# Kernel tuning notes

Measured on AMD Instinct MI355X. Metric: run time of the kernel, lower is better.

Reference implementation:

```python
import jax, jax.numpy as jnp
import numpy as np

N_NODES = 100000
N_EDGES = 1600000
N_FEAT = 128
HIDDEN = 128
N_CLASSES = 40


def gcn_conv(x, W, b, src, dst, norm, n):
    # PyG GCNConv: linear (no bias) -> gather src -> scale by sym norm -> scatter-add to dst -> + bias
    h = x @ W                      # [N, out]
    m = h[src] * norm[:, None]     # [E+N, out] gathered, normalized messages
    out = jax.ops.segment_sum(m, dst, num_segments=n)
    return out + b


def setup_inputs() -> dict:
    key = jax.random.key(0)
    ks = jax.random.split(key, 10)
    x = jax.random.normal(ks[0], (N_NODES, N_FEAT), dtype=jnp.float32)
    edge_index = jax.random.randint(ks[1], (2, N_EDGES), 0, N_NODES, dtype=jnp.int32)

    def lin(k, fan_in, fan_out):
        s = 1.0 / np.sqrt(fan_in)
        return (jax.random.uniform(k, (fan_in, fan_out), jnp.float32, -s, s))

    return {
        "x": x,
        "edge_index": edge_index,
        "W1": lin(ks[2], N_FEAT, HIDDEN), "b1": jnp.zeros((HIDDEN,), jnp.float32),
        "W2": lin(ks[3], HIDDEN, HIDDEN), "b2": jnp.zeros((HIDDEN,), jnp.float32),
        "W3": lin(ks[4], HIDDEN, HIDDEN), "b3": jnp.zeros((HIDDEN,), jnp.float32),
        "W4": lin(ks[5], HIDDEN, N_CLASSES), "b4": jnp.zeros((N_CLASSES,), jnp.float32),
    }


def reference(x, edge_index, W1, b1, W2, b2, W3, b3, W4, b4):
    n = x.shape[0]
    # add self-loops (PyG GCNConv default)
    loops = jnp.arange(n, dtype=edge_index.dtype)
    src = jnp.concatenate([edge_index[0], loops])
    dst = jnp.concatenate([edge_index[1], loops])
    # symmetric degree normalization: deg computed on destination index
    deg = jax.ops.segment_sum(jnp.ones_like(dst, x.dtype), dst, num_segments=n)
    dinv = jnp.where(deg > 0, jax.lax.rsqrt(deg), 0.0)
    norm = dinv[src] * dinv[dst]

    h = jax.nn.relu(gcn_conv(x, W1, b1, src, dst, norm, n))   # dropout = identity (eval)
    h = jax.nn.relu(gcn_conv(h, W2, b2, src, dst, norm, n))
    h = jax.nn.relu(gcn_conv(h, W3, b3, src, dst, norm, n))
    x_latent = h
    out = gcn_conv(h, W4, b4, src, dst, norm, n)
    return out, x_latent
```

## Files before the change

### kernel.cpp

```cpp
#include <hip/hip_runtime.h>
#include <hip/hip_bf16.h>
#include <hip/hip_fp16.h>


#define N_NODES 100000
#define N_EDGES 1600000

#define BSHIFT 7
#define BWIDTH 128
#define CELL_CAP 512
#define P1_EPT 16
#define P1_CHUNK 4096

typedef short s16x8 __attribute__((ext_vector_type(8)));
typedef _Float16 f16x8 __attribute__((ext_vector_type(8)));
typedef float f32x4 __attribute__((ext_vector_type(4)));
typedef float f32x2 __attribute__((ext_vector_type(2)));


__global__ void init_aux(int* __restrict__ bcur2, int* __restrict__ spillCnt, int m) {
    int i = blockIdx.x * blockDim.x + threadIdx.x;
    if (i < m) bcur2[i] = 0;
    if (i == 0) *spillCnt = 0;
}

__global__ __launch_bounds__(256) void pass1_bucket(const int* __restrict__ src,
                                                    const int* __restrict__ dst,
                                                    int* __restrict__ bcur2,
                                                    int2* __restrict__ cells,
                                                    int2* __restrict__ spill,
                                                    int* __restrict__ spillCnt,
                                                    int nb, int e) {
    __shared__ int hist[1024];
    __shared__ int base[1024];
    int t = threadIdx.x;
    int x = blockIdx.x & 7;
    int e0 = blockIdx.x * P1_CHUNK;

    for (int i = t; i < nb; i += 256) hist[i] = 0;
    __syncthreads();

    int ds[P1_EPT], ss[P1_EPT];
#pragma unroll
    for (int j = 0; j < P1_EPT; j++) {
        int i = e0 + j * 256 + t;
        if (i < e) {
            ds[j] = dst[i];
            ss[j] = src[i];
            atomicAdd(&hist[ds[j] >> BSHIFT], 1);
        } else {
            ds[j] = -1;
        }
    }
    __syncthreads();

    for (int i = t; i < nb; i += 256) {
        int h = hist[i];
        base[i] = (h > 0) ? atomicAdd(&bcur2[i * 8 + x], h) : 0;
        hist[i] = 0;
    }
    __syncthreads();

#pragma unroll
    for (int j = 0; j < P1_EPT; j++) {
        if (ds[j] >= 0) {
            int b = ds[j] >> BSHIFT;
            int r = atomicAdd(&hist[b], 1);
            int slot = base[b] + r;
            if (slot < CELL_CAP) {
                cells[(size_t)(b * 8 + x) * CELL_CAP + slot] = make_int2(ss[j], ds[j]);
            } else {
                int sp = atomicAdd(spillCnt, 1);
                spill[sp] = make_int2(ss[j], ds[j]);
            }
        }
    }
}

__global__ __launch_bounds__(256) void count_cells(const int* __restrict__ bcur2,
                                                   const int2* __restrict__ cells,
                                                   const int2* __restrict__ spill,
                                                   const int* __restrict__ spillCnt,
                                                   int* __restrict__ counts,
                                                   float* __restrict__ dinv,
                                                   int n) {
    __shared__ int cnt[BWIDTH];
    int b = blockIdx.x;
    int t = threadIdx.x;
    int nodeBase = b << BSHIFT;
    if (t < BWIDTH) cnt[t] = 0;
    __syncthreads();
    for (int x = 0; x < 8; x++) {
        int c = bcur2[b * 8 + x];
        if (c > CELL_CAP) c = CELL_CAP;
        const int2* cp = cells + (size_t)(b * 8 + x) * CELL_CAP;
        for (int s = t; s < c; s += 256) {
            atomicAdd(&cnt[cp[s].y - nodeBase], 1);
        }
    }
    int sc = *spillCnt;
    for (int s = t; s < sc; s += 256) {
        int d = spill[s].y;
        if ((d >> BSHIFT) == b) atomicAdd(&cnt[d - nodeBase], 1);
    }
    __syncthreads();
    if (t < BWIDTH) {
        int node = nodeBase + t;
        if (node < n) {
            int deg = cnt[t] + 1;
            counts[node] = deg;
            dinv[node] = 1.0f / sqrtf((float)deg);
        }
    }
}

__global__ __launch_bounds__(256) void scan_phase1(const int* __restrict__ counts,
                                                   int* __restrict__ blockSums, int n) {
    __shared__ int red[256];
    int t = threadIdx.x;
    int base = blockIdx.x * 1024 + t * 4;
    int s = 0;
    if (base + 3 < n) {
        int4 v = *(const int4*)(counts + base);
        s = ((v.x + 2) & ~3) + ((v.y + 2) & ~3) + ((v.z + 2) & ~3) + ((v.w + 2) & ~3);
    } else {
        for (int j = 0; j < 4; j++) if (base + j < n) s += (counts[base + j] + 2) & ~3;
    }
    red[t] = s;
    __syncthreads();
    for (int off = 128; off > 0; off >>= 1) {
        if (t < off) red[t] += red[t + off];
        __syncthreads();
    }
    if (t == 0) blockSums[blockIdx.x] = red[0];
}

__global__ __launch_bounds__(1024) void scan_phase2(int* __restrict__ blockSums, int nb) {
    __shared__ int sh[1024];
    int t = threadIdx.x;
    sh[t] = (t < nb) ? blockSums[t] : 0;
    __syncthreads();
    for (int off = 1; off < 1024; off <<= 1) {
        int v = (t >= off) ? sh[t - off] : 0;
        __syncthreads();
        sh[t] += v;
        __syncthreads();
    }
    if (t < nb) blockSums[t] = (t == 0) ? 0 : sh[t - 1];
}

__global__ __launch_bounds__(256) void scan_phase3(const int* __restrict__ counts,
                                                   const int* __restrict__ blockSums,
                                                   int* __restrict__ offsets, int n) {
    __shared__ int red[256];
    int t = threadIdx.x;
    int base = blockIdx.x * 1024 + t * 4;
    int c[4];
#pragma unroll
    for (int j = 0; j < 4; j++) c[j] = (base + j < n) ? ((counts[base + j] + 2) & ~3) : 0;
    int s = c[0] + c[1] + c[2] + c[3];
    red[t] = s;
    __syncthreads();
    for (int off = 1; off < 256; off <<= 1) {
        int v = (t >= off) ? red[t - off] : 0;
        __syncthreads();
        red[t] += v;
        __syncthreads();
    }
    int prefix = blockSums[blockIdx.x] + ((t == 0) ? 0 : red[t - 1]);
#pragma unroll
    for (int j = 0; j < 4; j++) {
        if (base + j < n) offsets[base + j] = prefix;
        prefix += c[j];
        if (base + j == n - 1) offsets[n] = prefix;
    }
}

__global__ void fill_pad(const int* __restrict__ counts, const int* __restrict__ offsets,
                         int* __restrict__ srcSorted, int n) {
    int i = blockIdx.x * blockDim.x + threadIdx.x;
    if (i < n) {
        int b = offsets[i] + counts[i] - 1;
        int e = offsets[i + 1];
        for (int k = b; k < e; k++) srcSorted[k] = n;
    }
}

__global__ __launch_bounds__(256) void pass2_scatter(const int* __restrict__ bcur2,
                                                     const int2* __restrict__ cells,
                                                     const int2* __restrict__ spill,
                                                     const int* __restrict__ spillCnt,
                                                     const int* __restrict__ offsets,
                                                     int* __restrict__ srcSorted) {
    __shared__ int cur[BWIDTH];
    int b = blockIdx.x;
    int t = threadIdx.x;
    int nodeBase = b << BSHIFT;
    if (t < BWIDTH) cur[t] = 0;
    __syncthreads();
    for (int x = 0; x < 8; x++) {
        int c = bcur2[b * 8 + x];
        if (c > CELL_CAP) c = CELL_CAP;
        const int2* cp = cells + (size_t)(b * 8 + x) * CELL_CAP;
        for (int s = t; s < c; s += 256) {
            int2 p = cp[s];
            int r = atomicAdd(&cur[p.y - nodeBase], 1);
            srcSorted[offsets[p.y] + r] = p.x;
        }
    }
    int sc = *spillCnt;
    for (int s = t; s < sc; s += 256) {
        int2 p = spill[s];
        if ((p.y >> BSHIFT) == b) {
            int r = atomicAdd(&cur[p.y - nodeBase], 1);
            srcSorted[offsets[p.y] + r] = p.x;
        }
    }
}


__device__ inline void split_bf16(float f, unsigned short& h, unsigned short& l) {
    unsigned u = __float_as_uint(f);
    unsigned hr = (u + 0x7FFFu + ((u >> 16) & 1u)) >> 16;
    h = (unsigned short)hr;
    float r = f - __uint_as_float(hr << 16);
    unsigned v = __float_as_uint(r);
    unsigned lr = (v + 0x7FFFu + ((v >> 16) & 1u)) >> 16;
    l = (unsigned short)lr;
}

__global__ __launch_bounds__(256) void prep_wfrag(const float* __restrict__ W,
                                                  short* __restrict__ wh,
                                                  short* __restrict__ wl,
                                                  __half* __restrict__ zrow) {
    if (zrow != nullptr && blockIdx.x == 0 && threadIdx.x < 64) {
        ((__half2*)zrow)[threadIdx.x] = __floats2half2_rn(0.f, 0.f);
    }
    int idx = blockIdx.x * 256 + threadIdx.x;
    int j    = idx & 7;
    int lane = (idx >> 3) & 63;
    int c    = (idx >> 9) & 3;
    int t    = idx >> 11;
    int quad = lane >> 4;
    int n = (t << 4) | (lane & 15);
    int k = (c << 5) + (quad << 3) + j;
    unsigned short h, l;
    split_bf16(W[k * 128 + n], h, l);
    wh[idx] = (short)h;
    wl[idx] = (short)l;
}

__global__ __launch_bounds__(256) void prep_wfrag16(const float* __restrict__ W,
                                                    _Float16* __restrict__ wh,
                                                    _Float16* __restrict__ wl) {
    int idx = blockIdx.x * 256 + threadIdx.x;
    int j    = idx & 7;
    int lane = (idx >> 3) & 63;
    int c    = (idx >> 9) & 3;
    int t    = idx >> 11;
    int quad = lane >> 4;
    int n = (t << 4) | (lane & 15);
    int k = (c << 5) + (quad << 3) + j;
    float v = W[k * 128 + n];
    _Float16 h = (_Float16)v;
    _Float16 l = (_Float16)((v - (float)h) * 2048.0f);
    wh[idx] = h;
    wl[idx] = l;
}


#define GEMM_GX 512

__global__ __launch_bounds__(256) void gemm_mfma(const float* __restrict__ A,
                                                 const short* __restrict__ wh,
                                                 const short* __restrict__ wl,
                                                 const float* __restrict__ dinv,
                                                 __half* __restrict__ C, int M) {
    int wv   = threadIdx.x >> 6;
    int lane = threadIdx.x & 63;
    int quad = lane >> 4;
    int mm   = lane & 15;
    int tbase = blockIdx.y * 4;

    s16x8 whf[4][4], wlf[4][4];
#pragma unroll
    for (int tt = 0; tt < 4; tt++)
#pragma unroll
        for (int c = 0; c < 4; c++) {
            int base = ((((tbase + tt) << 2) + c) << 6 | lane) << 3;
            whf[tt][c] = *(const s16x8*)(wh + base);
            wlf[tt][c] = *(const s16x8*)(wl + base);
        }

    int nStrips = M >> 4;
    for (int s = blockIdx.x * 4 + wv; s < nStrips; s += GEMM_GX * 4) {
        const float* ap = A + (size_t)((s << 4) + mm) * 128 + (quad << 3);
        f32x4 acc[4];
#pragma unroll
        for (int tt = 0; tt < 4; tt++) acc[tt] = (f32x4){0.f, 0.f, 0.f, 0.f};

#pragma unroll
        for (int c = 0; c < 4; c++) {
            float av[8];
            *(float4*)&av[0] = *(const float4*)(ap + (c << 5));
            *(float4*)&av[4] = *(const float4*)(ap + (c << 5) + 4);
            union { s16x8 v; unsigned short u[8]; } ah, al;
#pragma unroll
            for (int j = 0; j < 8; j++) split_bf16(av[j], ah.u[j], al.u[j]);
#pragma unroll
            for (int tt = 0; tt < 4; tt++) {
                acc[tt] = __builtin_amdgcn_mfma_f32_16x16x32_bf16(ah.v, whf[tt][c], acc[tt], 0, 0, 0);
                acc[tt] = __builtin_amdgcn_mfma_f32_16x16x32_bf16(ah.v, wlf[tt][c], acc[tt], 0, 0, 0);
                acc[tt] = __builtin_amdgcn_mfma_f32_16x16x32_bf16(al.v, whf[tt][c], acc[tt], 0, 0, 0);
                acc[tt] = __builtin_amdgcn_mfma_f32_16x16x32_bf16(al.v, wlf[tt][c], acc[tt], 0, 0, 0);
            }
        }
        int rbase = (s << 4) + (quad << 2);
        float dv[4];
#pragma unroll
        for (int r = 0; r < 4; r++) dv[r] = dinv[rbase + r];
        __half* cp = C + (size_t)rbase * 128 + (tbase << 4) + mm;
#pragma unroll
        for (int tt = 0; tt < 4; tt++) {
#pragma unroll
            for (int r = 0; r < 4; r++) {
                cp[(size_t)r * 128 + (tt << 4)] = __float2half(acc[tt][r] * dv[r]);
            }
        }
    }
}


__global__ __launch_bounds__(256) void gemm_mfma_f16(const __half* __restrict__ A,
                                                     const _Float16* __restrict__ wh,
                                                     const _Float16* __restrict__ wl,
                                                     const float* __restrict__ dinv,
                                                     __half* __restrict__ C, int M) {
    int wv   = threadIdx.x >> 6;
    int lane = threadIdx.x & 63;
    int quad = lane >> 4;
    int mm   = lane & 15;
    int tbase = blockIdx.y * 4;

    f16x8 whf[4][4], wlf[4][4];
#pragma unroll
    for (int tt = 0; tt < 4; tt++)
#pragma unroll
        for (int c = 0; c < 4; c++) {
            int base = ((((tbase + tt) << 2) + c) << 6 | lane) << 3;
            whf[tt][c] = *(const f16x8*)(wh + base);
            wlf[tt][c] = *(const f16x8*)(wl + base);
        }

    int nStrips = M >> 4;
    for (int s = blockIdx.x * 4 + wv; s < nStrips; s += GEMM_GX * 4) {
        const _Float16* ap = (const _Float16*)A + (size_t)((s << 4) + mm) * 128 + (quad << 3);
        f32x4 acch[4], accl[4];
#pragma unroll
        for (int tt = 0; tt < 4; tt++) {
            acch[tt] = (f32x4){0.f, 0.f, 0.f, 0.f};
            accl[tt] = (f32x4){0.f, 0.f, 0.f, 0.f};
        }

#pragma unroll
        for (int c = 0; c < 4; c++) {
            f16x8 av = *(const f16x8*)(ap + (c << 5));
#pragma unroll
            for (int tt = 0; tt < 4; tt++) {
                acch[tt] = __builtin_amdgcn_mfma_f32_16x16x32_f16(av, whf[tt][c], acch[tt], 0, 0, 0);
                accl[tt] = __builtin_amdgcn_mfma_f32_16x16x32_f16(av, wlf[tt][c], accl[tt], 0, 0, 0);
            }
        }
        int rbase = (s << 4) + (quad << 2);
        float dv[4];
#pragma unroll
        for (int r = 0; r < 4; r++) dv[r] = dinv[rbase + r];
        __half* cp = C + (size_t)rbase * 128 + (tbase << 4) + mm;
#pragma unroll
        for (int tt = 0; tt < 4; tt++) {
#pragma unroll
            for (int r = 0; r < 4; r++) {
                float v = acch[tt][r] + accl[tt][r] * (1.0f / 2048.0f);
                cp[(size_t)r * 128 + (tt << 4)] = __float2half(v * dv[r]);
            }
        }
    }
}


__global__ __launch_bounds__(320) void gemm_f32_40(const float* __restrict__ A,
                                                   const float* __restrict__ B,
                                                   const float* __restrict__ dinv,
                                                   __half* __restrict__ C, int M) {
    __shared__ float Ws[128][40];
    __shared__ float Xs[32][132];
    int t = threadIdx.x;
    int block_row = blockIdx.x * 32;

    for (int i = t; i < 128 * 40; i += 320) ((float*)Ws)[i] = B[i];
    for (int idx = t; idx < 1024; idx += 320) {
        int row = idx >> 5;
        int k4  = (idx & 31) << 2;
        int gr = block_row + row; if (gr >= M) gr = M - 1;
        float4 v = *(const float4*)(A + (size_t)gr * 128 + k4);
        *(float4*)&Xs[row][k4] = v;
    }
    __syncthreads();

    int r  = t / 10;
    int c0 = (t % 10) * 4;
    float4 acc = make_float4(0.f, 0.f, 0.f, 0.f);
    for (int k = 0; k < 128; k += 4) {
        float4 xv = *(const float4*)&Xs[r][k];
#pragma unroll
        for (int j = 0; j < 4; j++) {
            float xj = (j == 0) ? xv.x : (j == 1) ? xv.y : (j == 2) ? xv.z : xv.w;
            float4 wv = *(const float4*)&Ws[k + j][c0];
            acc.x += xj * wv.x; acc.y += xj * wv.y;
            acc.z += xj * wv.z; acc.w += xj * wv.w;
        }
    }
    int gr = block_row + r;
    if (gr < M) {
        float dv = dinv[gr];
        __half2* p = (__half2*)(C + (size_t)gr * 40 + c0);
        p[0] = __floats2half2_rn(dv * acc.x, dv * acc.y);
        p[1] = __floats2half2_rn(dv * acc.z, dv * acc.w);
    } else if (gr == M) {
        __half2* p = (__half2*)(C + (size_t)gr * 40 + c0);
        p[0] = __floats2half2_rn(0.f, 0.f);
        p[1] = __floats2half2_rn(0.f, 0.f);
    }
}


__device__ inline f32x2 h2f(__half2 v) {
    float2 t = __half22float2(v);
    return (f32x2){t.x, t.y};
}

template <int NF, bool RELU, typename OT>
__global__ __launch_bounds__(256) void agg_kernel(const __half* __restrict__ h,
                                                  const float* __restrict__ dinv,
                                                  const int* __restrict__ offsets,
                                                  const int* __restrict__ srcSorted,
                                                  const float* __restrict__ bias,
                                                  OT* __restrict__ out, int n) {
    int wave = threadIdx.x >> 6;
    int lane = threadIdx.x & 63;
    int node = blockIdx.x * 4 + wave;
    if (node >= n) return;

    int f = lane * 2;
    bool act = (f < NF);
    float di = dinv[node];
    const char* hb = (const char*)h;
    const unsigned RB = NF * 2;
    unsigned fb = (unsigned)f * 2;

    f32x2 a0 = (f32x2){0.f, 0.f}, a1 = a0, a2 = a0, a3 = a0;
    if (act) {
        a0 = h2f(*(const __half2*)(hb + (unsigned)node * RB + fb));
    }

    int idx = offsets[node];
    int end = offsets[node + 1];

    int4 sA, sB;
    bool have8 = (idx + 8 <= end);
    if (have8) {
        sA = *(const int4*)(srcSorted + idx);
        sB = *(const int4*)(srcSorted + idx + 4);
    }
    while (have8) {
        int4 cA = sA, cB = sB;
        int nidx = idx + 8;
        bool nxt = (nidx + 8 <= end);
        if (nxt) {
            sA = *(const int4*)(srcSorted + nidx);
            sB = *(const int4*)(srcSorted + nidx + 4);
        }
        if (act) {
            __half2 v0 = *(const __half2*)(hb + (unsigned)cA.x * RB + fb);
            __half2 v1 = *(const __half2*)(hb + (unsigned)cA.y * RB + fb);
            __half2 v2 = *(const __half2*)(hb + (unsigned)cA.z * RB + fb);
            __half2 v3 = *(const __half2*)(hb + (unsigned)cA.w * RB + fb);
            __half2 v4 = *(const __half2*)(hb + (unsigned)cB.x * RB + fb);
            __half2 v5 = *(const __half2*)(hb + (unsigned)cB.y * RB + fb);
            __half2 v6 = *(const __half2*)(hb + (unsigned)cB.z * RB + fb);
            __half2 v7 = *(const __half2*)(hb + (unsigned)cB.w * RB + fb);
            a0 += h2f(v0); a1 += h2f(v1); a2 += h2f(v2); a3 += h2f(v3);
            a0 += h2f(v4); a1 += h2f(v5); a2 += h2f(v6); a3 += h2f(v7);
        }
        idx = nidx;
        have8 = nxt;
    }
    if (idx + 4 <= end) {
        int4 cA = *(const int4*)(srcSorted + idx);
        if (act) {
            __half2 v0 = *(const __half2*)(hb + (unsigned)cA.x * RB + fb);
            __half2 v1 = *(const __half2*)(hb + (unsigned)cA.y * RB + fb);
            __half2 v2 = *(const __half2*)(hb + (unsigned)cA.z * RB + fb);
            __half2 v3 = *(const __half2*)(hb + (unsigned)cA.w * RB + fb);
            a0 += h2f(v0); a1 += h2f(v1); a2 += h2f(v2); a3 += h2f(v3);
        }
    }

    if (act) {
        f32x2 s = (a0 + a1) + (a2 + a3);
        float ox = di * s.x + bias[f];
        float oy = di * s.y + bias[f + 1];
        if (RELU) { ox = fmaxf(ox, 0.f); oy = fmaxf(oy, 0.f); }
        if constexpr (sizeof(OT) == 2) {
            *(__half2*)(out + (size_t)node * NF + f) = __floats2half2_rn(ox, oy);
        } else {
            *(float2*)(out + (size_t)node * NF + f) = make_float2(ox, oy);
        }
    }
}


extern "C" void kernel_launch(void* const* d_in, const int* in_sizes, int n_in,
                              void* d_out, int out_size, void* d_ws, size_t ws_size,
                              hipStream_t stream) {
    const float* x  = (const float*)d_in[0];
    const int* edge = (const int*)d_in[1];
    const float* W1 = (const float*)d_in[2]; const float* b1 = (const float*)d_in[3];
    const float* W2 = (const float*)d_in[4]; const float* b2 = (const float*)d_in[5];
    const float* W3 = (const float*)d_in[6]; const float* b3 = (const float*)d_in[7];
    const float* W4 = (const float*)d_in[8]; const float* b4 = (const float*)d_in[9];

    const int N = in_sizes[0] / 128;
    const int E = in_sizes[1] / 2;
    const int* src = edge;
    const int* dst = edge + E;

    float* out_final = (float*)d_out;
    float* x_latent  = (float*)d_out + (size_t)N * 40;

    const int nbk = (N + BWIDTH - 1) >> BSHIFT;

    char* w = (char*)d_ws;
    int* counts    = (int*)w;  w += (size_t)N * 4;
    int* offsets   = (int*)w;  w += (size_t)(N + 4) * 4;
    float* dinv    = (float*)w; w += (size_t)N * 4;
    int* srcSorted = (int*)w;  w += (size_t)(E + 4 * N) * 4;
    int* blockSums = (int*)w;  w += (size_t)1024 * 4;
    int* bcur2     = (int*)w;  w += (size_t)8448 * 4;
    int* spillCnt  = (int*)w;  w += (size_t)64 * 4;
    short* wfrag   = (short*)w;    w += (size_t)2 * 16384 * 2;
    _Float16* wf16 = (_Float16*)w; w += (size_t)4 * 16384 * 2;
    w = (char*)(((uintptr_t)w + 255) & ~(uintptr_t)255);
    __half* hA   = (__half*)w; w += (size_t)(N + 1) * 128 * 2;
    __half* hB16 = (__half*)w; w += (size_t)N * 128 * 2;

    int2* cells = (int2*)hA;
    int2* spill = cells + (size_t)nbk * 8 * CELL_CAP;

    short* wh1 = wfrag;            short* wl1 = wfrag + 16384;
    _Float16* wh2 = wf16;          _Float16* wl2 = wf16 + 16384;
    _Float16* wh3 = wf16 + 32768;  _Float16* wl3 = wf16 + 49152;

    int gN = (N + 255) / 256;
    int nb = (N + 1023) / 1024;
    int p1b = (E + P1_CHUNK - 1) / P1_CHUNK;

    init_aux<<<(nbk * 8 + 255) / 256, 256, 0, stream>>>(bcur2, spillCnt, nbk * 8);
    pass1_bucket<<<p1b, 256, 0, stream>>>(src, dst, bcur2, cells, spill, spillCnt, nbk, E);
    count_cells<<<nbk, 256, 0, stream>>>(bcur2, cells, spill, spillCnt, counts, dinv, N);
    scan_phase1<<<nb, 256, 0, stream>>>(counts, blockSums, N);
    scan_phase2<<<1, 1024, 0, stream>>>(blockSums, nb);
    scan_phase3<<<nb, 256, 0, stream>>>(counts, blockSums, offsets, N);
    fill_pad<<<gN, 256, 0, stream>>>(counts, offsets, srcSorted, N);
    pass2_scatter<<<nbk, 256, 0, stream>>>(bcur2, cells, spill, spillCnt, offsets, srcSorted);

    prep_wfrag<<<64, 256, 0, stream>>>(W1, wh1, wl1, hA + (size_t)N * 128);
    prep_wfrag16<<<64, 256, 0, stream>>>(W2, wh2, wl2);
    prep_wfrag16<<<64, 256, 0, stream>>>(W3, wh3, wl3);

    dim3 gGemm(GEMM_GX, 2);
    int gAgg = (N + 3) / 4;

    gemm_mfma<<<gGemm, 256, 0, stream>>>(x, wh1, wl1, dinv, hA, N);
    agg_kernel<128, true, __half><<<gAgg, 256, 0, stream>>>(hA, dinv, offsets, srcSorted, b1, hB16, N);
    gemm_mfma_f16<<<gGemm, 256, 0, stream>>>(hB16, wh2, wl2, dinv, hA, N);
    agg_kernel<128, true, __half><<<gAgg, 256, 0, stream>>>(hA, dinv, offsets, srcSorted, b2, hB16, N);
    gemm_mfma_f16<<<gGemm, 256, 0, stream>>>(hB16, wh3, wl3, dinv, hA, N);
    agg_kernel<128, true, float><<<gAgg, 256, 0, stream>>>(hA, dinv, offsets, srcSorted, b3, x_latent, N);
    gemm_f32_40<<<(N + 1 + 31) / 32, 320, 0, stream>>>(x_latent, W4, dinv, hA, N);
    agg_kernel<40, false, float><<<gAgg, 256, 0, stream>>>(hA, dinv, offsets, srcSorted, b4, out_final, N);
}
```

Baseline: 500.3 us.

## Aggregate two nodes per wave for 128-wide layers and three for 40-wide

The aggregation kernel is split in two. The 128-feature layers now process two destination nodes per wave with interleaved gather loops, which doubles the loads in flight. The 40-class layer packs three nodes into one wave using 20-lane subgroups, so far fewer lanes sit idle. Both use a fixed grid-stride launch of 2048 blocks instead of one block per four nodes. This adds register pressure and some divergence when neighbour counts differ, and relies on the padded CSR layout (multiples of 4).

```diff
diff --git a/kernel.cpp b/kernel.cpp
--- a/kernel.cpp
+++ b/kernel.cpp
@@ -439,82 +439,174 @@
     return (f32x2){t.x, t.y};
 }
 
-template <int NF, bool RELU, typename OT>
-__global__ __launch_bounds__(256) void agg_kernel(const __half* __restrict__ h,
-                                                  const float* __restrict__ dinv,
-                                                  const int* __restrict__ offsets,
-                                                  const int* __restrict__ srcSorted,
-                                                  const float* __restrict__ bias,
-                                                  OT* __restrict__ out, int n) {
+template <bool RELU, typename OT>
+__global__ __launch_bounds__(256) void agg128_pair(const __half* __restrict__ h,
+                                                   const float* __restrict__ dinv,
+                                                   const int* __restrict__ offsets,
+                                                   const int* __restrict__ srcSorted,
+                                                   const float* __restrict__ bias,
+                                                   OT* __restrict__ out, int n) {
     int wave = threadIdx.x >> 6;
     int lane = threadIdx.x & 63;
-    int node = blockIdx.x * 4 + wave;
-    if (node >= n) return;
-
     int f = lane * 2;
-    bool act = (f < NF);
-    float di = dinv[node];
+    unsigned fb = (unsigned)f * 2u;
     const char* hb = (const char*)h;
-    const unsigned RB = NF * 2;
-    unsigned fb = (unsigned)f * 2;
-
-    f32x2 a0 = (f32x2){0.f, 0.f}, a1 = a0, a2 = a0, a3 = a0;
-    if (act) {
-        a0 = h2f(*(const __half2*)(hb + (unsigned)node * RB + fb));
-    }
-
-    int idx = offsets[node];
-    int end = offsets[node + 1];
-
-    int4 sA, sB;
-    bool have8 = (idx + 8 <= end);
-    if (have8) {
-        sA = *(const int4*)(srcSorted + idx);
-        sB = *(const int4*)(srcSorted + idx + 4);
-    }
-    while (have8) {
-        int4 cA = sA, cB = sB;
-        int nidx = idx + 8;
-        bool nxt = (nidx + 8 <= end);
-        if (nxt) {
-            sA = *(const int4*)(srcSorted + nidx);
-            sB = *(const int4*)(srcSorted + nidx + 4);
-        }
-        if (act) {
-            __half2 v0 = *(const __half2*)(hb + (unsigned)cA.x * RB + fb);
-            __half2 v1 = *(const __half2*)(hb + (unsigned)cA.y * RB + fb);
-            __half2 v2 = *(const __half2*)(hb + (unsigned)cA.z * RB + fb);
-            __half2 v3 = *(const __half2*)(hb + (unsigned)cA.w * RB + fb);
-            __half2 v4 = *(const __half2*)(hb + (unsigned)cB.x * RB + fb);
-            __half2 v5 = *(const __half2*)(hb + (unsigned)cB.y * RB + fb);
-            __half2 v6 = *(const __half2*)(hb + (unsigned)cB.z * RB + fb);
-            __half2 v7 = *(const __half2*)(hb + (unsigned)cB.w * RB + fb);
-            a0 += h2f(v0); a1 += h2f(v1); a2 += h2f(v2); a3 += h2f(v3);
-            a0 += h2f(v4); a1 += h2f(v5); a2 += h2f(v6); a3 += h2f(v7);
-        }
-        idx = nidx;
-        have8 = nxt;
-    }
-    if (idx + 4 <= end) {
-        int4 cA = *(const int4*)(srcSorted + idx);
-        if (act) {
-            __half2 v0 = *(const __half2*)(hb + (unsigned)cA.x * RB + fb);
-            __half2 v1 = *(const __half2*)(hb + (unsigned)cA.y * RB + fb);
-            __half2 v2 = *(const __half2*)(hb + (unsigned)cA.z * RB + fb);
-            __half2 v3 = *(const __half2*)(hb + (unsigned)cA.w * RB + fb);
-            a0 += h2f(v0); a1 += h2f(v1); a2 += h2f(v2); a3 += h2f(v3);
-        }
-    }
-
-    if (act) {
-        f32x2 s = (a0 + a1) + (a2 + a3);
-        float ox = di * s.x + bias[f];
-        float oy = di * s.y + bias[f + 1];
-        if (RELU) { ox = fmaxf(ox, 0.f); oy = fmaxf(oy, 0.f); }
-        if constexpr (sizeof(OT) == 2) {
-            *(__half2*)(out + (size_t)node * NF + f) = __floats2half2_rn(ox, oy);
-        } else {
-            *(float2*)(out + (size_t)node * NF + f) = make_float2(ox, oy);
+    float bx = bias[f], by = bias[f + 1];
+    int npairs = (n + 1) >> 1;
+
+    for (int p = blockIdx.x * 4 + wave; p < npairs; p += gridDim.x * 4) {
+        int n0 = p * 2;
+        int n1 = n0 + 1;
+        bool has1 = (n1 < n);
+        int2 oo = *(const int2*)(offsets + n0);
+        int e1 = has1 ? offsets[n0 + 2] : oo.y;
+        float di0 = dinv[n0];
+        float di1 = has1 ? dinv[n1] : 0.f;
+
+        f32x2 z = (f32x2){0.f, 0.f};
+        f32x2 A0 = h2f(*(const __half2*)(hb + (unsigned)n0 * 256u + fb));
+        f32x2 A1 = z, A2 = z, A3 = z;
+        f32x2 B0 = z, B1 = z, B2 = z, B3 = z;
+        if (has1) B0 = h2f(*(const __half2*)(hb + (unsigned)n1 * 256u + fb));
+
+        int i0 = oo.x, e0 = oo.y, i1 = oo.y;
+        bool c0 = (i0 + 8 <= e0), c1 = (i1 + 8 <= e1);
+        while (c0 || c1) {
+            int4 sA0, sB0, sA1, sB1;
+            if (c0) { sA0 = *(const int4*)(srcSorted + i0); sB0 = *(const int4*)(srcSorted + i0 + 4); }
+            if (c1) { sA1 = *(const int4*)(srcSorted + i1); sB1 = *(const int4*)(srcSorted + i1 + 4); }
+            __half2 v0, v1, v2, v3, v4, v5, v6, v7;
+            __half2 w0, w1, w2, w3, w4, w5, w6, w7;
+            if (c0) {
+                v0 = *(const __half2*)(hb + (unsigned)sA0.x * 256u + fb);
+                v1 = *(const __half2*)(hb + (unsigned)sA0.y * 256u + fb);
+                v2 = *(const __half2*)(hb + (unsigned)sA0.z * 256u + fb);
+                v3 = *(const __half2*)(hb + (unsigned)sA0.w * 256u + fb);
+                v4 = *(const __half2*)(hb + (unsigned)sB0.x * 256u + fb);
+                v5 = *(const __half2*)(hb + (unsigned)sB0.y * 256u + fb);
+                v6 = *(const __half2*)(hb + (unsigned)sB0.z * 256u + fb);
+                v7 = *(const __half2*)(hb + (unsigned)sB0.w * 256u + fb);
+            }
+            if (c1) {
+                w0 = *(const __half2*)(hb + (unsigned)sA1.x * 256u + fb);
+                w1 = *(const __half2*)(hb + (unsigned)sA1.y * 256u + fb);
+                w2 = *(const __half2*)(hb + (unsigned)sA1.z * 256u + fb);
+                w3 = *(const __half2*)(hb + (unsigned)sA1.w * 256u + fb);
+                w4 = *(const __half2*)(hb + (unsigned)sB1.x * 256u + fb);
+                w5 = *(const __half2*)(hb + (unsigned)sB1.y * 256u + fb);
+                w6 = *(const __half2*)(hb + (unsigned)sB1.z * 256u + fb);
+                w7 = *(const __half2*)(hb + (unsigned)sB1.w * 256u + fb);
+            }
+            if (c0) {
+                A0 += h2f(v0); A1 += h2f(v1); A2 += h2f(v2); A3 += h2f(v3);
+                A0 += h2f(v4); A1 += h2f(v5); A2 += h2f(v6); A3 += h2f(v7);
+                i0 += 8;
+            }
+            if (c1) {
+                B0 += h2f(w0); B1 += h2f(w1); B2 += h2f(w2); B3 += h2f(w3);
+                B0 += h2f(w4); B1 += h2f(w5); B2 += h2f(w6); B3 += h2f(w7);
+                i1 += 8;
+            }
+            c0 = (i0 + 8 <= e0); c1 = (i1 + 8 <= e1);
+        }
+        if (i0 + 4 <= e0) {
+            int4 s = *(const int4*)(srcSorted + i0);
+            A0 += h2f(*(const __half2*)(hb + (unsigned)s.x * 256u + fb));
+            A1 += h2f(*(const __half2*)(hb + (unsigned)s.y * 256u + fb));
+            A2 += h2f(*(const __half2*)(hb + (unsigned)s.z * 256u + fb));
+            A3 += h2f(*(const __half2*)(hb + (unsigned)s.w * 256u + fb));
+        }
+        if (i1 + 4 <= e1) {
+            int4 s = *(const int4*)(srcSorted + i1);
+            B0 += h2f(*(const __half2*)(hb + (unsigned)s.x * 256u + fb));
+            B1 += h2f(*(const __half2*)(hb + (unsigned)s.y * 256u + fb));
+            B2 += h2f(*(const __half2*)(hb + (unsigned)s.z * 256u + fb));
+            B3 += h2f(*(const __half2*)(hb + (unsigned)s.w * 256u + fb));
+        }
+
+        {
+            f32x2 s = (A0 + A1) + (A2 + A3);
+            float ox = di0 * s.x + bx;
+            float oy = di0 * s.y + by;
+            if (RELU) { ox = fmaxf(ox, 0.f); oy = fmaxf(oy, 0.f); }
+            if constexpr (sizeof(OT) == 2) {
+                *(__half2*)(out + (size_t)n0 * 128 + f) = __floats2half2_rn(ox, oy);
+            } else {
+                *(float2*)(out + (size_t)n0 * 128 + f) = make_float2(ox, oy);
+            }
+        }
+        if (has1) {
+            f32x2 s = (B0 + B1) + (B2 + B3);
+            float ox = di1 * s.x + bx;
+            float oy = di1 * s.y + by;
+            if (RELU) { ox = fmaxf(ox, 0.f); oy = fmaxf(oy, 0.f); }
+            if constexpr (sizeof(OT) == 2) {
+                *(__half2*)(out + (size_t)n1 * 128 + f) = __floats2half2_rn(ox, oy);
+            } else {
+                *(float2*)(out + (size_t)n1 * 128 + f) = make_float2(ox, oy);
+            }
+        }
+    }
+}
+
+__global__ __launch_bounds__(256) void agg40_tri(const __half* __restrict__ h,
+                                                 const float* __restrict__ dinv,
+                                                 const int* __restrict__ offsets,
+                                                 const int* __restrict__ srcSorted,
+                                                 const float* __restrict__ bias,
+                                                 float* __restrict__ out, int n) {
+    int wave = threadIdx.x >> 6;
+    int lane = threadIdx.x & 63;
+    unsigned sub = (unsigned)lane / 20u;
+    int fi = lane - (int)sub * 20;
+    bool act = (sub < 3u);
+    int f = fi * 2;
+    unsigned fb = (unsigned)fi * 4u;
+    const char* hb = (const char*)h;
+    float bx = act ? bias[f] : 0.f;
+    float by = act ? bias[f + 1] : 0.f;
+    int ntri = (n + 2) / 3;
+
+    for (int p = blockIdx.x * 4 + wave; p < ntri; p += gridDim.x * 4) {
+        int node = p * 3 + (int)sub;
+        bool on = act && (node < n);
+        float di = on ? dinv[node] : 0.f;
+        int idx = on ? offsets[node] : 0;
+        int end = on ? offsets[node + 1] : 0;
+
+        f32x2 z = (f32x2){0.f, 0.f};
+        f32x2 a0 = z, a1 = z, a2 = z, a3 = z;
+        if (on) a0 = h2f(*(const __half2*)(hb + (unsigned)node * 80u + fb));
+
+        while (__any(idx + 8 <= end)) {
+            bool c = (idx + 8 <= end);
+            if (c) {
+                int4 sA = *(const int4*)(srcSorted + idx);
+                int4 sB = *(const int4*)(srcSorted + idx + 4);
+                a0 += h2f(*(const __half2*)(hb + (unsigned)sA.x * 80u + fb));
+                a1 += h2f(*(const __half2*)(hb + (unsigned)sA.y * 80u + fb));
+                a2 += h2f(*(const __half2*)(hb + (unsigned)sA.z * 80u + fb));
+                a3 += h2f(*(const __half2*)(hb + (unsigned)sA.w * 80u + fb));
+                a0 += h2f(*(const __half2*)(hb + (unsigned)sB.x * 80u + fb));
+                a1 += h2f(*(const __half2*)(hb + (unsigned)sB.y * 80u + fb));
+                a2 += h2f(*(const __half2*)(hb + (unsigned)sB.z * 80u + fb));
+                a3 += h2f(*(const __half2*)(hb + (unsigned)sB.w * 80u + fb));
+                idx += 8;
+            }
+        }
+        if (idx + 4 <= end) {
+            int4 sA = *(const int4*)(srcSorted + idx);
+            a0 += h2f(*(const __half2*)(hb + (unsigned)sA.x * 80u + fb));
+            a1 += h2f(*(const __half2*)(hb + (unsigned)sA.y * 80u + fb));
+            a2 += h2f(*(const __half2*)(hb + (unsigned)sA.z * 80u + fb));
+            a3 += h2f(*(const __half2*)(hb + (unsigned)sA.w * 80u + fb));
+        }
+
+        if (on) {
+            f32x2 s = (a0 + a1) + (a2 + a3);
+            float ox = di * s.x + bx;
+            float oy = di * s.y + by;
+            *(float2*)(out + (size_t)node * 40 + f) = make_float2(ox, oy);
         }
     }
 }
@@ -579,14 +671,14 @@
     prep_wfrag16<<<64, 256, 0, stream>>>(W3, wh3, wl3);
 
     dim3 gGemm(GEMM_GX, 2);
-    int gAgg = (N + 3) / 4;
+    int gAgg = 2048;
 
     gemm_mfma<<<gGemm, 256, 0, stream>>>(x, wh1, wl1, dinv, hA, N);
-    agg_kernel<128, true, __half><<<gAgg, 256, 0, stream>>>(hA, dinv, offsets, srcSorted, b1, hB16, N);
+    agg128_pair<true, __half><<<gAgg, 256, 0, stream>>>(hA, dinv, offsets, srcSorted, b1, hB16, N);
     gemm_mfma_f16<<<gGemm, 256, 0, stream>>>(hB16, wh2, wl2, dinv, hA, N);
-    agg_kernel<128, true, __half><<<gAgg, 256, 0, stream>>>(hA, dinv, offsets, srcSorted, b2, hB16, N);
+    agg128_pair<true, __half><<<gAgg, 256, 0, stream>>>(hA, dinv, offsets, srcSorted, b2, hB16, N);
     gemm_mfma_f16<<<gGemm, 256, 0, stream>>>(hB16, wh3, wl3, dinv, hA, N);
-    agg_kernel<128, true, float><<<gAgg, 256, 0, stream>>>(hA, dinv, offsets, srcSorted, b3, x_latent, N);
+    agg128_pair<true, float><<<gAgg, 256, 0, stream>>>(hA, dinv, offsets, srcSorted, b3, x_latent, N);
     gemm_f32_40<<<(N + 1 + 31) / 32, 320, 0, stream>>>(x_latent, W4, dinv, hA, N);
-    agg_kernel<40, false, float><<<gAgg, 256, 0, stream>>>(hA, dinv, offsets, srcSorted, b4, out_final, N);
-}
+    agg40_tri<<<gAgg, 256, 0, stream>>>(hA, dinv, offsets, srcSorted, b4, out_final, N);
+}
```

Measured after the change: 513.4 us. 2.6% more time.

## Fold pad fill into scatter, memset aux, and pack three nodes per wave in final aggregation

Applied to the files above, without the earlier changes.

The separate fill_pad kernel is removed. Each pass2_scatter block now pads its own nodes' unused CSR slots after the scatter, using its shared per-node counters. The init kernel becomes a hipMemsetAsync. The 40-feature final aggregation moves to a new persistent kernel that packs three nodes into each 64-lane wave (20 lanes each, 60 lanes active) instead of leaving most lanes idle. The goals are fewer launches and better lane use in the last layer; the cost is the added padding loop in scatter and the wave-wide __any loop, which makes each wave wait for the longest of its three nodes.

```diff
diff --git a/kernel.cpp b/kernel.cpp
--- a/kernel.cpp
+++ b/kernel.cpp
@@ -17,12 +17,6 @@
 typedef float f32x4 __attribute__((ext_vector_type(4)));
 typedef float f32x2 __attribute__((ext_vector_type(2)));
 
-
-__global__ void init_aux(int* __restrict__ bcur2, int* __restrict__ spillCnt, int m) {
-    int i = blockIdx.x * blockDim.x + threadIdx.x;
-    if (i < m) bcur2[i] = 0;
-    if (i == 0) *spillCnt = 0;
-}
 
 __global__ __launch_bounds__(256) void pass1_bucket(const int* __restrict__ src,
                                                     const int* __restrict__ dst,
@@ -176,22 +170,12 @@
     }
 }
 
-__global__ void fill_pad(const int* __restrict__ counts, const int* __restrict__ offsets,
-                         int* __restrict__ srcSorted, int n) {
-    int i = blockIdx.x * blockDim.x + threadIdx.x;
-    if (i < n) {
-        int b = offsets[i] + counts[i] - 1;
-        int e = offsets[i + 1];
-        for (int k = b; k < e; k++) srcSorted[k] = n;
-    }
-}
-
 __global__ __launch_bounds__(256) void pass2_scatter(const int* __restrict__ bcur2,
                                                      const int2* __restrict__ cells,
                                                      const int2* __restrict__ spill,
                                                      const int* __restrict__ spillCnt,
                                                      const int* __restrict__ offsets,
-                                                     int* __restrict__ srcSorted) {
+                                                     int* __restrict__ srcSorted, int n) {
     __shared__ int cur[BWIDTH];
     int b = blockIdx.x;
     int t = threadIdx.x;
@@ -214,6 +198,15 @@
         if ((p.y >> BSHIFT) == b) {
             int r = atomicAdd(&cur[p.y - nodeBase], 1);
             srcSorted[offsets[p.y] + r] = p.x;
+        }
+    }
+    __syncthreads();
+    if (t < BWIDTH) {
+        int node = nodeBase + t;
+        if (node < n) {
+            int beg = offsets[node] + cur[t];
+            int end = offsets[node + 1];
+            for (int k = beg; k < end; k++) srcSorted[k] = n;
         }
     }
 }
@@ -519,6 +512,68 @@
     }
 }
 
+__global__ __launch_bounds__(256) void agg40_tri(const __half* __restrict__ h,
+                                                 const float* __restrict__ dinv,
+                                                 const int* __restrict__ offsets,
+                                                 const int* __restrict__ srcSorted,
+                                                 const float* __restrict__ bias,
+                                                 float* __restrict__ out, int n) {
+    int wave = threadIdx.x >> 6;
+    int lane = threadIdx.x & 63;
+    unsigned sub = (unsigned)lane / 20u;
+    int fi = lane - (int)sub * 20;
+    bool act = (sub < 3u);
+    int f = fi * 2;
+    unsigned fb = (unsigned)fi * 4u;
+    const char* hb = (const char*)h;
+    float bx = act ? bias[f] : 0.f;
+    float by = act ? bias[f + 1] : 0.f;
+    int ntri = (n + 2) / 3;
+
+    for (int p = blockIdx.x * 4 + wave; p < ntri; p += gridDim.x * 4) {
+        int node = p * 3 + (int)sub;
+        bool on = act && (node < n);
+        float di = on ? dinv[node] : 0.f;
+        int idx = on ? offsets[node] : 0;
+        int end = on ? offsets[node + 1] : 0;
+
+        f32x2 z = (f32x2){0.f, 0.f};
+        f32x2 a0 = z, a1 = z, a2 = z, a3 = z;
+        if (on) a0 = h2f(*(const __half2*)(hb + (unsigned)node * 80u + fb));
+
+        while (__any(idx + 8 <= end)) {
+            bool c = (idx + 8 <= end);
+            if (c) {
+                int4 sA = *(const int4*)(srcSorted + idx);
+                int4 sB = *(const int4*)(srcSorted + idx + 4);
+                a0 += h2f(*(const __half2*)(hb + (unsigned)sA.x * 80u + fb));
+                a1 += h2f(*(const __half2*)(hb + (unsigned)sA.y * 80u + fb));
+                a2 += h2f(*(const __half2*)(hb + (unsigned)sA.z * 80u + fb));
+                a3 += h2f(*(const __half2*)(hb + (unsigned)sA.w * 80u + fb));
+                a0 += h2f(*(const __half2*)(hb + (unsigned)sB.x * 80u + fb));
+                a1 += h2f(*(const __half2*)(hb + (unsigned)sB.y * 80u + fb));
+                a2 += h2f(*(const __half2*)(hb + (unsigned)sB.z * 80u + fb));
+                a3 += h2f(*(const __half2*)(hb + (unsigned)sB.w * 80u + fb));
+                idx += 8;
+            }
+        }
+        if (idx + 4 <= end) {
+            int4 sA = *(const int4*)(srcSorted + idx);
+            a0 += h2f(*(const __half2*)(hb + (unsigned)sA.x * 80u + fb));
+            a1 += h2f(*(const __half2*)(hb + (unsigned)sA.y * 80u + fb));
+            a2 += h2f(*(const __half2*)(hb + (unsigned)sA.z * 80u + fb));
+            a3 += h2f(*(const __half2*)(hb + (unsigned)sA.w * 80u + fb));
+        }
+
+        if (on) {
+            f32x2 s = (a0 + a1) + (a2 + a3);
+            float ox = di * s.x + bx;
+            float oy = di * s.y + by;
+            *(float2*)(out + (size_t)node * 40 + f) = make_float2(ox, oy);
+        }
+    }
+}
+
 
 extern "C" void kernel_launch(void* const* d_in, const int* in_sizes, int n_in,
                               void* d_out, int out_size, void* d_ws, size_t ws_size,
@@ -561,18 +616,16 @@
     _Float16* wh2 = wf16;          _Float16* wl2 = wf16 + 16384;
     _Float16* wh3 = wf16 + 32768;  _Float16* wl3 = wf16 + 49152;
 
-    int gN = (N + 255) / 256;
     int nb = (N + 1023) / 1024;
     int p1b = (E + P1_CHUNK - 1) / P1_CHUNK;
 
-    init_aux<<<(nbk * 8 + 255) / 256, 256, 0, stream>>>(bcur2, spillCnt, nbk * 8);
+    hipMemsetAsync(bcur2, 0, (size_t)(8448 + 64) * 4, stream);
     pass1_bucket<<<p1b, 256, 0, stream>>>(src, dst, bcur2, cells, spill, spillCnt, nbk, E);
     count_cells<<<nbk, 256, 0, stream>>>(bcur2, cells, spill, spillCnt, counts, dinv, N);
     scan_phase1<<<nb, 256, 0, stream>>>(counts, blockSums, N);
     scan_phase2<<<1, 1024, 0, stream>>>(blockSums, nb);
     scan_phase3<<<nb, 256, 0, stream>>>(counts, blockSums, offsets, N);
-    fill_pad<<<gN, 256, 0, stream>>>(counts, offsets, srcSorted, N);
-    pass2_scatter<<<nbk, 256, 0, stream>>>(bcur2, cells, spill, spillCnt, offsets, srcSorted);
+    pass2_scatter<<<nbk, 256, 0, stream>>>(bcur2, cells, spill, spillCnt, offsets, srcSorted, N);
 
     prep_wfrag<<<64, 256, 0, stream>>>(W1, wh1, wl1, hA + (size_t)N * 128);
     prep_wfrag16<<<64, 256, 0, stream>>>(W2, wh2, wl2);
@@ -588,5 +641,5 @@
     gemm_mfma_f16<<<gGemm, 256, 0, stream>>>(hB16, wh3, wl3, dinv, hA, N);
     agg_kernel<128, true, float><<<gAgg, 256, 0, stream>>>(hA, dinv, offsets, srcSorted, b3, x_latent, N);
     gemm_f32_40<<<(N + 1 + 31) / 32, 320, 0, stream>>>(x_latent, W4, dinv, hA, N);
-    agg_kernel<40, false, float><<<gAgg, 256, 0, stream>>>(hA, dinv, offsets, srcSorted, b4, out_final, N);
-}
+    agg40_tri<<<2048, 256, 0, stream>>>(hA, dinv, offsets, srcSorted, b4, out_final, N);
+}
```

After: 486.0 us. 2.9% less time.
